# Kernel tuning notes

Measured on AMD Instinct MI355X. Metric: run time of the kernel, lower is better.

The kernel has to match this reference:

```python
import jax, jax.numpy as jnp
import numpy as np

B, C, K, P, STRIDE, ITERS = 32, 32, 3, 4, 1, 3
PSIZE = P * P
EPS = 1e-6


def unfold_patches(x, K, stride):
    # Replicates F.unfold(x_chw, kernel_size=K, padding=K//2, stride=stride)
    # followed by transpose(1,2).view(b, oh, ow, K*K, c) — including the
    # channel-major flat ordering that the view reinterprets.
    b, h, w, c = x.shape
    pad = K // 2
    xp = jnp.pad(jnp.transpose(x, (0, 3, 1, 2)), ((0, 0), (0, 0), (pad, pad), (pad, pad)))
    oh = (h + 2 * pad - K) // stride + 1
    ow = (w + 2 * pad - K) // stride + 1
    rows = []
    for ki in range(K):
        cols = []
        for kj in range(K):
            cols.append(xp[:, :, ki:ki + (oh - 1) * stride + 1:stride, kj:kj + (ow - 1) * stride + 1:stride])
        rows.append(jnp.stack(cols, axis=2))  # (b, c, K, oh, ow)
    pat = jnp.stack(rows, axis=2)  # (b, c, K, K, oh, ow)
    pat = pat.reshape(b, c * K * K, oh * ow)  # unfold output (b, c*K*K, L)
    pat = jnp.transpose(pat, (0, 2, 1)).reshape(b, oh, ow, K * K, c)
    return pat, oh, ow


def squash(s, eps=EPS):
    s2 = jnp.sum(s * s, axis=-1, keepdims=True)
    return (s2 / (1.0 + s2)) * s / jnp.sqrt(s2 + eps)


def dynamic_routing(v, a_in, iters=ITERS, eps=EPS):
    # v: (n, in_votes, C, psize), a_in: (n, in_votes, 1)
    n, in_votes, Cc, _ = v.shape
    b_ij = jnp.zeros((n, in_votes, Cc), dtype=v.dtype)
    a_in = jnp.clip(a_in, 0.0001, 1.0)
    v_j = None
    for t in range(iters):
        c_ij = jax.nn.softmax(b_ij, axis=2) * a_in
        c_ij = c_ij / (jnp.sum(c_ij, axis=2, keepdims=True) + eps)
        s_j = jnp.einsum('nic,nicq->ncq', c_ij, v)
        v_j = squash(s_j)
        if t < iters - 1:
            agreement = jnp.einsum('nicq,ncq->nic', v, v_j)
            b_ij = b_ij + agreement
    a_out = jnp.clip(jnp.sqrt(jnp.sum(v_j * v_j, axis=-1) + eps), 0.0001, 1.0 - 0.0001)
    return v_j, a_out


def setup_inputs() -> dict:
    key = jax.random.key(0)
    k1, k2 = jax.random.split(key)
    x = jax.random.normal(k1, (2, 14, 14, B * (PSIZE + 1)), dtype=jnp.float32)
    weights = jax.random.normal(k2, (K * K * B, C, PSIZE, PSIZE), dtype=jnp.float32) * 0.02
    return {"x": x, "weights": weights}


def reference(x, weights):
    b, h, w, c = x.shape
    patches, oh, ow = unfold_patches(x, K, STRIDE)
    p_in = patches[..., :B * PSIZE].reshape(b * oh * ow, K * K * B, PSIZE)
    a_in = patches[..., B * PSIZE:].reshape(b * oh * ow, K * K * B, 1)
    votes = jnp.einsum('bip,icpq->bicq', p_in, weights)  # (n, KKB, C, psize)
    p_vec, a_vec = dynamic_routing(votes, a_in)
    p_out = p_vec.reshape(b, oh, ow, C * PSIZE)
    a_out = a_vec.reshape(b, oh, ow, C)
    out = jnp.concatenate([p_out, a_out], axis=3)
    p_out = jnp.nan_to_num(p_out, nan=0.0, posinf=10000.0, neginf=-10000.0)
    a_out = jnp.nan_to_num(a_out, nan=0.5, posinf=1.0 - 0.0001, neginf=0.0001)
    out = jnp.nan_to_num(out, nan=0.0, posinf=10000.0, neginf=-10000.0)
    return p_out, a_out, out
```

## Files before the change

### kernel.cpp

```cpp
#include <hip/hip_runtime.h>
#include <hip/hip_fp16.h>
#include <math.h>

#define NB 392
#define NI 288
#define NC 32
#define NQ 16
#define CQ 512
#define CH 544
#define EPSV 1e-6f
#define NPAD 448

#define VSCALE 32.0f
#define VINV (1.0f / 32.0f)

#define P16E (NI*NPAD*16)
#define W16E (NI*CQ*16)
#define AFACE (NB*NI)

#define OFF_AFAC 0
#define OFF_P16  (AFACE)
#define OFF_W16  (OFF_P16 + P16E/2)
#define OFF_VOT  (OFF_W16 + W16E/2)

#define OFF_AOUT 200704
#define OFF_CAT  213248

#define RT_THREADS 512
#define RT_WAVES 8

#define PW_BLOCKS (NI*2)
#define P16_BLOCKS (P16E/8/256)
#define AFAC_BLOCKS ((AFACE+255)/256)

typedef _Float16 v4h __attribute__((ext_vector_type(4)));
typedef float v4f __attribute__((ext_vector_type(4)));
typedef float v2f __attribute__((ext_vector_type(2)));

__device__ __forceinline__ float gather_x(const float* __restrict__ x, int n, int j) {
    int c_idx = j / 9;
    int rem = j - c_idx * 9;
    int ki = rem / 3;
    int kj = rem - ki * 3;
    int b_ = n / 196;
    int rest = n - b_ * 196;
    int yy = rest / 14;
    int xx = rest - yy * 14;
    int iy = yy + ki - 1;
    int ix = xx + kj - 1;
    float v = 0.f;
    if ((unsigned)iy < 14u && (unsigned)ix < 14u)
        v = x[((b_ * 14 + iy) * 14 + ix) * CH + c_idx];
    return v;
}

__global__ __launch_bounds__(256) void prep_k(const float* __restrict__ x,
                                              const float* __restrict__ wts,
                                              ushort* __restrict__ p16,
                                              ushort* __restrict__ w16,
                                              float* __restrict__ afac) {
    __shared__ float wl[4096];
    int b = blockIdx.x;
    int t = threadIdx.x;

    if (b < PW_BLOCKS) {
        int i = b >> 1, h = b & 1;
        const float4* src = (const float4*)(wts + (size_t)i * 8192 + h * 4096);
#pragma unroll
        for (int it = 0; it < 4; ++it)
            *(float4*)&wl[(it * 256 + t) * 4] = src[it * 256 + t];
        __syncthreads();
        uint4* dst = (uint4*)(w16 + (size_t)i * 8192 + h * 4096);
#pragma unroll
        for (int it = 0; it < 2; ++it) {
            int idx = it * 256 + t;
            int cl = idx >> 1;
            int m = idx & 1;
            int base = (cl >> 4) * 256 + (cl & 15);
            uint v[4];
#pragma unroll
            for (int kk = 0; kk < 4; ++kk) {
                __half2 hh = __floats2half2_rn(wl[base + (8 * m + 2 * kk) * 16],
                                               wl[base + (8 * m + 2 * kk + 1) * 16]);
                v[kk] = *(uint*)&hh;
            }
            dst[cl * 2 + m] = make_uint4(v[0], v[1], v[2], v[3]);
        }
    } else if (b < PW_BLOCKS + P16_BLOCKS) {
        int idx = (b - PW_BLOCKS) * 256 + t;
        int half = idx & 1;
        int r = idx >> 1;
        int n = r % NPAD;
        int i = r / NPAD;
        uint4 val = {0u, 0u, 0u, 0u};
        if (n < NB) {
            int jb = (i >> 5) * CH + (i & 31) * 16 + half * 8;
            uint v[4];
#pragma unroll
            for (int kk = 0; kk < 4; ++kk) {
                __half2 hh = __floats2half2_rn(gather_x(x, n, jb + 2 * kk),
                                               gather_x(x, n, jb + 2 * kk + 1));
                v[kk] = *(uint*)&hh;
            }
            val = make_uint4(v[0], v[1], v[2], v[3]);
        }
        *(uint4*)(p16 + (size_t)idx * 8) = val;
    } else {
        int t3 = (b - PW_BLOCKS - P16_BLOCKS) * 256 + t;
        if (t3 < AFACE) {
            int i = t3 % NI;
            int n = t3 / NI;
            int j = (i >> 5) * CH + 512 + (i & 31);
            float v = gather_x(x, n, j);
            float a = fminf(fmaxf(v, 1e-4f), 1.0f);
            afac[t3] = a / (a + EPSV);
        }
    }
}

__global__ __launch_bounds__(256) void votes_k(const ushort* __restrict__ p16,
                                               const ushort* __restrict__ w16,
                                               uchar* __restrict__ votes) {
    __shared__ uchar tile[64 * 144];
    int mtt = blockIdx.x;
    int i = blockIdx.y;
    int t = threadIdx.x;
    int wv = t >> 6;
    int l = t & 63;
    int col = l & 15;
    int quad = l >> 4;

    int row_a = mtt * 64 + wv * 16 + col;
    v4h av = *(const v4h*)(p16 + ((size_t)(i * NPAD + row_a) << 4) + (quad << 2));

    for (int ch = 0; ch < 4; ++ch) {
#pragma unroll
        for (int c8 = 0; c8 < 8; ++c8) {
            int ct = ch * 8 + c8;
            v4h bv = *(const v4h*)(w16 + ((size_t)(i * CQ + ct * 16 + col) << 4) + (quad << 2));
            v4f acc = {0.f, 0.f, 0.f, 0.f};
            acc = __builtin_amdgcn_mfma_f32_16x16x16f16(av, bv, acc, 0, 0, 0);
            uint u01 = __builtin_amdgcn_cvt_pk_fp8_f32(acc[0] * VSCALE, acc[1] * VSCALE, 0, false);
            uint u23 = __builtin_amdgcn_cvt_pk_fp8_f32(acc[2] * VSCALE, acc[3] * VSCALE, 0, false);
            uchar* tb = &tile[(wv * 16 + quad * 4) * 144 + c8 * 16 + col];
            tb[0 * 144] = (uchar)(u01 & 0xFF);
            tb[1 * 144] = (uchar)((u01 >> 8) & 0xFF);
            tb[2 * 144] = (uchar)(u23 & 0xFF);
            tb[3 * 144] = (uchar)((u23 >> 8) & 0xFF);
        }
        __syncthreads();
#pragma unroll
        for (int k = 0; k < 2; ++k) {
            int idx = k * 256 + t;
            int row = idx >> 3;
            int off = idx & 7;
            int n_out = mtt * 64 + row;
            if (n_out < NB) {
                uint4 d = *(const uint4*)&tile[row * 144 + off * 16];
                *(uint4*)(votes + (((size_t)n_out * NI + i) << 9) + ch * 128 + off * 16) = d;
            }
        }
        __syncthreads();
    }
}

__global__ __launch_bounds__(RT_THREADS) void routing_k(const uchar* __restrict__ votes,
                                                        const float* __restrict__ afac,
                                                        float* __restrict__ out) {
    __shared__ float afs[NI];
    __shared__ float sred[RT_WAVES * CQ];
    __shared__ float vj[CQ];
    __shared__ float aout_s[NC];

    int n = blockIdx.x;
    int t = threadIdx.x;
    int wv = t >> 6;
    int l = t & 63;
    int c = l & 31;
    int g = l >> 5;

    if (t < NI) afs[t] = afac[n * NI + t];
    __syncthreads();

    const uchar* vb = votes + (size_t)n * NI * 512;
    float vjr[16];
    float sreg[16];

#define VROW(S) (((const uint4*)(vb + ((size_t)(((((S) << 3) + wv) << 1) + g) << 9)))[c])

    for (int iter = 0; iter < 3; ++iter) {
#pragma unroll
        for (int q = 0; q < 16; ++q) sreg[q] = 0.f;

        uint4 f0 = VROW(0), f1 = VROW(1), f2 = VROW(2);

#pragma clang loop unroll_count(2)
        for (int s = 0; s < 18; ++s) {
            int i = ((s << 3) + wv) * 2 + g;
            uint4 cur = f0;
            f0 = f1; f1 = f2;
            if (s + 3 < 18) f2 = VROW(s + 3);

            float vt[16];
            {
                v2f p;
                p = __builtin_amdgcn_cvt_pk_f32_fp8(cur.x, false); vt[0] = p[0];  vt[1] = p[1];
                p = __builtin_amdgcn_cvt_pk_f32_fp8(cur.x, true);  vt[2] = p[0];  vt[3] = p[1];
                p = __builtin_amdgcn_cvt_pk_f32_fp8(cur.y, false); vt[4] = p[0];  vt[5] = p[1];
                p = __builtin_amdgcn_cvt_pk_f32_fp8(cur.y, true);  vt[6] = p[0];  vt[7] = p[1];
                p = __builtin_amdgcn_cvt_pk_f32_fp8(cur.z, false); vt[8] = p[0];  vt[9] = p[1];
                p = __builtin_amdgcn_cvt_pk_f32_fp8(cur.z, true);  vt[10] = p[0]; vt[11] = p[1];
                p = __builtin_amdgcn_cvt_pk_f32_fp8(cur.w, false); vt[12] = p[0]; vt[13] = p[1];
                p = __builtin_amdgcn_cvt_pk_f32_fp8(cur.w, true);  vt[14] = p[0]; vt[15] = p[1];
            }
            float cij;
            if (iter == 0) {
                cij = afs[i] * (1.0f / 32.0f);
            } else {
                float ah = 0.f;
#pragma unroll
                for (int q = 0; q < 16; ++q) ah += vt[q] * vjr[q];
                float e = __expf(ah);
                float ssum = e;
                ssum += __shfl_xor(ssum, 1);
                ssum += __shfl_xor(ssum, 2);
                ssum += __shfl_xor(ssum, 4);
                ssum += __shfl_xor(ssum, 8);
                ssum += __shfl_xor(ssum, 16);
                cij = e * __builtin_amdgcn_rcpf(ssum) * afs[i];
            }
#pragma unroll
            for (int q = 0; q < 16; ++q) sreg[q] += cij * vt[q];
        }

#pragma unroll
        for (int q = 0; q < 16; ++q) sreg[q] += __shfl_xor(sreg[q], 32);
        if (g == 0) {
            float* sw = &sred[wv * CQ + c];
#pragma unroll
            for (int q = 0; q < 16; ++q) sw[q * 32] = sreg[q];
        }
        __syncthreads();
        {
            float ssum = 0.f;
#pragma unroll
            for (int k = 0; k < RT_WAVES; ++k) ssum += sred[k * CQ + t];
            sred[t] = ssum * VINV;
        }
        __syncthreads();

        if (t < NC) {
            float s2 = 0.f;
#pragma unroll
            for (int q = 0; q < 16; ++q) {
                float s = sred[q * 32 + t];
                s2 += s * s;
            }
            float f = (s2 / (1.f + s2)) / sqrtf(s2 + EPSV);
            float vn2 = 0.f;
#pragma unroll
            for (int q = 0; q < 16; ++q) {
                float v = f * sred[q * 32 + t];
                vj[q * 32 + t] = v;
                vn2 += v * v;
            }
            if (iter == 2) {
                float ao = sqrtf(vn2 + EPSV);
                ao = fminf(fmaxf(ao, 1e-4f), 1.f - 1e-4f);
                aout_s[t] = ao;
            }
        }
        __syncthreads();
        if (iter < 2) {
#pragma unroll
            for (int q = 0; q < 16; ++q) {
                float v = vj[q * 32 + c] * VINV;
                vjr[q] = (iter == 0) ? v : vjr[q] + v;
            }
        }
    }

    {
        float v = vj[(t & 15) * 32 + (t >> 4)];
        out[(size_t)n * CQ + t] = v;
        out[OFF_CAT + (size_t)n * 544 + t] = v;
    }
    if (t < NC) {
        float ao = aout_s[t];
        out[OFF_AOUT + n * 32 + t] = ao;
        out[OFF_CAT + (size_t)n * 544 + 512 + t] = ao;
    }
}

extern "C" void kernel_launch(void* const* d_in, const int* in_sizes, int n_in,
                              void* d_out, int out_size, void* d_ws, size_t ws_size,
                              hipStream_t stream) {
    const float* x = (const float*)d_in[0];
    const float* wts = (const float*)d_in[1];
    float* out = (float*)d_out;
    float* ws = (float*)d_ws;

    float* afac = ws + OFF_AFAC;
    ushort* p16 = (ushort*)(ws + OFF_P16);
    ushort* w16 = (ushort*)(ws + OFF_W16);
    uchar* votes = (uchar*)(ws + OFF_VOT);

    hipLaunchKernelGGL(prep_k, dim3(PW_BLOCKS + P16_BLOCKS + AFAC_BLOCKS), dim3(256), 0, stream,
                       x, wts, p16, w16, afac);
    hipLaunchKernelGGL(votes_k, dim3(7, NI), dim3(256), 0, stream,
                       p16, w16, votes);
    hipLaunchKernelGGL(routing_k, dim3(NB), dim3(RT_THREADS), 0, stream,
                       votes, afac, out);
}
```

Before: 118.1 us.

## Fuse prep kernel into votes and routing kernels, removing fp16 staging buffers

Drops the separate prep kernel. The votes kernel now converts its weight slice to fp16 into LDS and gathers the patch inputs directly from x. The routing kernel computes the activation factors inline from x. This removes one launch and the workspace round trip for p16, w16 and afac. In exchange, each of the 7 row-tile blocks per capsule re-reads and re-converts the same 32KB of weights, and scattered gather_x loads now sit on the votes kernel's critical path.

```diff
diff --git a/kernel.cpp b/kernel.cpp
--- a/kernel.cpp
+++ b/kernel.cpp
@@ -9,29 +9,15 @@
 #define CQ 512
 #define CH 544
 #define EPSV 1e-6f
-#define NPAD 448
 
 #define VSCALE 32.0f
 #define VINV (1.0f / 32.0f)
 
-#define P16E (NI*NPAD*16)
-#define W16E (NI*CQ*16)
-#define AFACE (NB*NI)
-
-#define OFF_AFAC 0
-#define OFF_P16  (AFACE)
-#define OFF_W16  (OFF_P16 + P16E/2)
-#define OFF_VOT  (OFF_W16 + W16E/2)
-
 #define OFF_AOUT 200704
 #define OFF_CAT  213248
 
 #define RT_THREADS 512
 #define RT_WAVES 8
-
-#define PW_BLOCKS (NI*2)
-#define P16_BLOCKS (P16E/8/256)
-#define AFAC_BLOCKS ((AFACE+255)/256)
 
 typedef _Float16 v4h __attribute__((ext_vector_type(4)));
 typedef float v4f __attribute__((ext_vector_type(4)));
@@ -54,73 +40,10 @@
     return v;
 }
 
-__global__ __launch_bounds__(256) void prep_k(const float* __restrict__ x,
-                                              const float* __restrict__ wts,
-                                              ushort* __restrict__ p16,
-                                              ushort* __restrict__ w16,
-                                              float* __restrict__ afac) {
-    __shared__ float wl[4096];
-    int b = blockIdx.x;
-    int t = threadIdx.x;
-
-    if (b < PW_BLOCKS) {
-        int i = b >> 1, h = b & 1;
-        const float4* src = (const float4*)(wts + (size_t)i * 8192 + h * 4096);
-#pragma unroll
-        for (int it = 0; it < 4; ++it)
-            *(float4*)&wl[(it * 256 + t) * 4] = src[it * 256 + t];
-        __syncthreads();
-        uint4* dst = (uint4*)(w16 + (size_t)i * 8192 + h * 4096);
-#pragma unroll
-        for (int it = 0; it < 2; ++it) {
-            int idx = it * 256 + t;
-            int cl = idx >> 1;
-            int m = idx & 1;
-            int base = (cl >> 4) * 256 + (cl & 15);
-            uint v[4];
-#pragma unroll
-            for (int kk = 0; kk < 4; ++kk) {
-                __half2 hh = __floats2half2_rn(wl[base + (8 * m + 2 * kk) * 16],
-                                               wl[base + (8 * m + 2 * kk + 1) * 16]);
-                v[kk] = *(uint*)&hh;
-            }
-            dst[cl * 2 + m] = make_uint4(v[0], v[1], v[2], v[3]);
-        }
-    } else if (b < PW_BLOCKS + P16_BLOCKS) {
-        int idx = (b - PW_BLOCKS) * 256 + t;
-        int half = idx & 1;
-        int r = idx >> 1;
-        int n = r % NPAD;
-        int i = r / NPAD;
-        uint4 val = {0u, 0u, 0u, 0u};
-        if (n < NB) {
-            int jb = (i >> 5) * CH + (i & 31) * 16 + half * 8;
-            uint v[4];
-#pragma unroll
-            for (int kk = 0; kk < 4; ++kk) {
-                __half2 hh = __floats2half2_rn(gather_x(x, n, jb + 2 * kk),
-                                               gather_x(x, n, jb + 2 * kk + 1));
-                v[kk] = *(uint*)&hh;
-            }
-            val = make_uint4(v[0], v[1], v[2], v[3]);
-        }
-        *(uint4*)(p16 + (size_t)idx * 8) = val;
-    } else {
-        int t3 = (b - PW_BLOCKS - P16_BLOCKS) * 256 + t;
-        if (t3 < AFACE) {
-            int i = t3 % NI;
-            int n = t3 / NI;
-            int j = (i >> 5) * CH + 512 + (i & 31);
-            float v = gather_x(x, n, j);
-            float a = fminf(fmaxf(v, 1e-4f), 1.0f);
-            afac[t3] = a / (a + EPSV);
-        }
-    }
-}
-
-__global__ __launch_bounds__(256) void votes_k(const ushort* __restrict__ p16,
-                                               const ushort* __restrict__ w16,
+__global__ __launch_bounds__(256) void votes_k(const float* __restrict__ x,
+                                               const float* __restrict__ wts,
                                                uchar* __restrict__ votes) {
+    __shared__ ushort w16l[8192];
     __shared__ uchar tile[64 * 144];
     int mtt = blockIdx.x;
     int i = blockIdx.y;
@@ -130,14 +53,38 @@
     int col = l & 15;
     int quad = l >> 4;
 
-    int row_a = mtt * 64 + wv * 16 + col;
-    v4h av = *(const v4h*)(p16 + ((size_t)(i * NPAD + row_a) << 4) + (quad << 2));
+    {
+        const float4* src = (const float4*)(wts + (size_t)i * 8192);
+#pragma unroll
+        for (int it = 0; it < 8; ++it) {
+            float4 f4 = src[it * 256 + t];
+            int fidx = (it * 256 + t) * 4;
+            int c = fidx >> 8;
+            int p = (fidx >> 4) & 15;
+            int q0 = fidx & 15;
+            ushort* wb = &w16l[(c * 16 + q0) * 16 + p];
+            wb[0]  = __half_as_ushort(__float2half(f4.x));
+            wb[16] = __half_as_ushort(__float2half(f4.y));
+            wb[32] = __half_as_ushort(__float2half(f4.z));
+            wb[48] = __half_as_ushort(__float2half(f4.w));
+        }
+    }
+
+    int n_row = mtt * 64 + wv * 16 + col;
+    v4h av = {};
+    if (n_row < NB) {
+        int jb = (i >> 5) * CH + (i & 31) * 16 + quad * 4;
+#pragma unroll
+        for (int kk = 0; kk < 4; ++kk)
+            av[kk] = (_Float16)gather_x(x, n_row, jb + kk);
+    }
+    __syncthreads();
 
     for (int ch = 0; ch < 4; ++ch) {
 #pragma unroll
         for (int c8 = 0; c8 < 8; ++c8) {
             int ct = ch * 8 + c8;
-            v4h bv = *(const v4h*)(w16 + ((size_t)(i * CQ + ct * 16 + col) << 4) + (quad << 2));
+            v4h bv = *(const v4h*)&w16l[(ct * 16 + col) * 16 + quad * 4];
             v4f acc = {0.f, 0.f, 0.f, 0.f};
             acc = __builtin_amdgcn_mfma_f32_16x16x16f16(av, bv, acc, 0, 0, 0);
             uint u01 = __builtin_amdgcn_cvt_pk_fp8_f32(acc[0] * VSCALE, acc[1] * VSCALE, 0, false);
@@ -165,7 +112,7 @@
 }
 
 __global__ __launch_bounds__(RT_THREADS) void routing_k(const uchar* __restrict__ votes,
-                                                        const float* __restrict__ afac,
+                                                        const float* __restrict__ x,
                                                         float* __restrict__ out) {
     __shared__ float afs[NI];
     __shared__ float sred[RT_WAVES * CQ];
@@ -179,7 +126,12 @@
     int c = l & 31;
     int g = l >> 5;
 
-    if (t < NI) afs[t] = afac[n * NI + t];
+    if (t < NI) {
+        int j = (t >> 5) * CH + 512 + (t & 31);
+        float v = gather_x(x, n, j);
+        float a = fminf(fmaxf(v, 1e-4f), 1.0f);
+        afs[t] = a / (a + EPSV);
+    }
     __syncthreads();
 
     const uchar* vb = votes + (size_t)n * NI * 512;
@@ -298,17 +250,10 @@
     const float* x = (const float*)d_in[0];
     const float* wts = (const float*)d_in[1];
     float* out = (float*)d_out;
-    float* ws = (float*)d_ws;
-
-    float* afac = ws + OFF_AFAC;
-    ushort* p16 = (ushort*)(ws + OFF_P16);
-    ushort* w16 = (ushort*)(ws + OFF_W16);
-    uchar* votes = (uchar*)(ws + OFF_VOT);
-
-    hipLaunchKernelGGL(prep_k, dim3(PW_BLOCKS + P16_BLOCKS + AFAC_BLOCKS), dim3(256), 0, stream,
-                       x, wts, p16, w16, afac);
+    uchar* votes = (uchar*)d_ws;
+
     hipLaunchKernelGGL(votes_k, dim3(7, NI), dim3(256), 0, stream,
-                       p16, w16, votes);
+                       x, wts, votes);
     hipLaunchKernelGGL(routing_k, dim3(NB), dim3(RT_THREADS), 0, stream,
-                       votes, afac, out);
-}
+                       votes, x, out);
+}
```

New measurement: 120.4 us. About the same (+2.0%).
